# Performance work log

Measured on AMD Instinct MI355X. Metric: run time of the kernel, lower is better.

Reference implementation:

```python
import jax, jax.numpy as jnp
import numpy as np

B, D, F = 2048, 512, 16384
K = 3
AUX_THR = 0.7
EPS = 1e-8


def setup_inputs() -> dict:
    key = jax.random.key(0)
    ks = jax.random.split(key, 14)
    sc_e = 1.0 / np.sqrt(D)
    sc_d = 1.0 / np.sqrt(F)
    return {
        "model_activations": jax.random.normal(ks[0], (B, D), jnp.float32),
        "We": jax.random.normal(ks[1], (F, D), jnp.float32) * sc_e,
        "be": jax.random.normal(ks[2], (F,), jnp.float32) * 0.01,
        "Wd": jax.random.normal(ks[3], (D, F), jnp.float32) * sc_d,
        "bd": jax.random.normal(ks[4], (D,), jnp.float32) * 0.01,
        "We1": jax.random.normal(ks[5], (F, D), jnp.float32) * sc_e,
        "be1": jax.random.normal(ks[6], (F,), jnp.float32) * 0.01,
        "Wd1": jax.random.normal(ks[7], (D, F), jnp.float32) * sc_d,
        "bd1": jax.random.normal(ks[8], (D,), jnp.float32) * 0.01,
        "We2": jax.random.normal(ks[9], (F, D), jnp.float32) * sc_e,
        "be2": jax.random.normal(ks[10], (F,), jnp.float32) * 0.01,
        "Wd2": jax.random.normal(ks[11], (D, F), jnp.float32) * sc_d,
        "bd2": jax.random.normal(ks[12], (D,), jnp.float32) * 0.01,
    }


def _forward(x, We, be, Wd, bd, We1, be1, Wd1, bd1, We2, be2, Wd2, bd2):
    # parent encoder + top-k scatter
    pre = x @ We.T + be                                   # [B, F]
    vals, idx = jax.lax.top_k(pre, K)                     # [B, K]
    sae = jnp.zeros_like(pre).at[jnp.arange(B)[:, None], idx].set(vals)

    # child routing
    pre1 = x @ We1.T + be1
    pre2 = x @ We2.T + be2
    sae_nz = sae != 0.0
    m1 = jnp.where(sae_nz, pre1, 0.0)
    m2 = jnp.where(sae_nz, pre2, 0.0)
    winners = m1 > m2
    fa1 = jnp.where(winners, m1, 0.0)
    fa2 = jnp.where(~winners, m2, 0.0)

    recon = (sae @ Wd.T + bd) + (fa1 @ Wd1.T + bd1) + (fa2 @ Wd2.T + bd2)

    # live-latent counts (as arrays, jit-friendly)
    n_parent = jnp.zeros((F,), jnp.float32).at[idx.reshape(-1)].set(1.0).sum().astype(jnp.int32)
    n_c1 = jnp.any(fa1 != 0, axis=0).sum().astype(jnp.int32)
    n_c2 = jnp.any(fa2 != 0, axis=0).sum().astype(jnp.int32)

    # auxiliary cosine loss, computed per-feature without materializing
    # the [B, D, F] scaled_parent / combined_weights tensors:
    #   scaled_parent[b,:,f] = a * Wd[:,f],  scaled_child[b,:,f] = c * Wc[:,f]
    # cos over D reduces to per-feature Gram terms.
    pp = jnp.sum(Wd * Wd, axis=0)      # [F] ||Wp_f||^2
    p1 = jnp.sum(Wd * Wd1, axis=0)     # [F] Wp_f . W1_f
    p2 = jnp.sum(Wd * Wd2, axis=0)
    s11 = jnp.sum(Wd1 * Wd1, axis=0)
    s22 = jnp.sum(Wd2 * Wd2, axis=0)

    a = sae                                              # [B, F]
    c = jnp.where(winners, fa1, fa2)                     # [B, F]
    pc = jnp.where(winners, p1[None, :], p2[None, :])    # [B, F]
    cc = jnp.where(winners, s11[None, :], s22[None, :])

    dot = a * (a * pp[None, :] + c * pc)                 # <scaled_parent, combined>
    nx = jnp.abs(a) * jnp.sqrt(pp)[None, :]              # ||scaled_parent||
    ny2 = a * a * pp[None, :] + 2.0 * a * c * pc + c * c * cc
    ny = jnp.sqrt(jnp.maximum(ny2, 0.0))                 # ||combined||
    cos = dot / (jnp.maximum(nx, EPS) * jnp.maximum(ny, EPS))

    active = (a > 0).astype(cos.dtype)
    sim_loss = jnp.maximum(0.0, AUX_THR - cos) * active
    aux = sim_loss.sum() / (active.sum() + 1e-08)

    return recon, (n_parent, n_c1, n_c2), aux


def reference(model_activations, We, be, Wd, bd, We1, be1, Wd1, bd1, We2, be2, Wd2, bd2):
    return _forward(model_activations, We, be, Wd, bd, We1, be1, Wd1, bd1, We2, be2, Wd2, bd2)
```

## Files before the change

kernel.cpp:

```cpp
#include <hip/hip_runtime.h>
#include <math.h>

#define B_DIM 2048
#define D_DIM 512
#define F_DIM 16384
#define K_TOP 3

typedef __attribute__((ext_vector_type(8))) short bf16x8;
typedef __attribute__((ext_vector_type(4))) float f32x4;

#define GL16(gsrc, ldst) \
  __builtin_amdgcn_global_load_lds( \
      (__attribute__((address_space(1))) const void*)(gsrc), \
      (__attribute__((address_space(3))) void*)(ldst), 16, 0, 0)

__device__ __forceinline__ bool better(float v, int c, float w, int j) {
    return (v > w) || (v == w && c < j);
}

__device__ __forceinline__ void ins3(float v, int c,
    float& v0, int& i0, float& v1, int& i1, float& v2, int& i2)
{
    if (!better(v, c, v2, i2)) return;
    if (better(v, c, v1, i1)) {
        v2 = v1; i2 = i1;
        if (better(v, c, v0, i0)) { v1 = v0; i1 = i0; v0 = v; i0 = c; }
        else { v1 = v; i1 = c; }
    } else { v2 = v; i2 = c; }
}

__device__ __forceinline__ uint okey(uint b16, int col) {
    uint m = 0x8000u + ((b16 >> 15) * 0x7FFFu);
    return ((b16 ^ m) << 14) | (uint)(16383 - col);
}

__device__ __forceinline__ void insK8(uint k, uint* V) {
#pragma unroll
    for (int j = 0; j < 8; ++j) {
        uint hi = V[j] > k ? V[j] : k;
        uint lo = V[j] > k ? k : V[j];
        V[j] = hi; k = lo;
    }
}

__device__ __forceinline__ void insK3(uint k, uint& V0, uint& V1, uint& V2) {
    uint h0 = V0 > k ? V0 : k, l0 = V0 > k ? k : V0; V0 = h0; k = l0;
    uint h1 = V1 > k ? V1 : k, l1 = V1 > k ? k : V1; V1 = h1; k = l1;
    V2 = V2 > k ? V2 : k;
}

__global__ __launch_bounds__(256) void convert_kernel(
    const float* __restrict__ src, ushort* __restrict__ dst, int n8)
{
    int i = blockIdx.x * 256 + threadIdx.x;
    const int stride = gridDim.x * 256;
    for (; i < n8; i += stride) {
        float4 a = ((const float4*)src)[i * 2];
        float4 b = ((const float4*)src)[i * 2 + 1];
        uint4 o;
        o.x = (__float_as_uint(a.y) & 0xFFFF0000u) | (__float_as_uint(a.x) >> 16);
        o.y = (__float_as_uint(a.w) & 0xFFFF0000u) | (__float_as_uint(a.z) >> 16);
        o.z = (__float_as_uint(b.y) & 0xFFFF0000u) | (__float_as_uint(b.x) >> 16);
        o.w = (__float_as_uint(b.w) & 0xFFFF0000u) | (__float_as_uint(b.z) >> 16);
        ((uint4*)dst)[i] = o;
    }
}

__global__ __launch_bounds__(256) void gemm_kernel(
    const ushort* __restrict__ xb, const ushort* __restrict__ web,
    const float* __restrict__ be, uint* __restrict__ packed)
{
    __shared__ __align__(16) ushort As[2][4096];
    __shared__ __align__(16) ushort Bs[2][4096];

    const int t = threadIdx.x;
    const int l = t & 63;
    const int w = t >> 6;
    const int wr = w >> 1, wc = w & 1;
    const int bm0 = blockIdx.y << 7;
    const int fn0 = blockIdx.x << 7;
    const int frow = l & 15;
    const int q = l >> 4;

    const int srow = t >> 2;
    const int sgr = (t & 3) ^ ((t >> 3) & 3);
    const int soff = sgr << 3;
    const ushort* gA0 = xb + (size_t)(bm0 + srow) * D_DIM + soff;
    const ushort* gA1 = xb + (size_t)(bm0 + 64 + srow) * D_DIM + soff;
    const ushort* gB0 = web + (size_t)(fn0 + srow) * D_DIM + soff;
    const ushort* gB1 = web + (size_t)(fn0 + 64 + srow) * D_DIM + soff;

#define STAGE(bufp, koff) do { \
    GL16(gA0 + (koff), (char*)As + (bufp) * 8192 + t * 16); \
    GL16(gA1 + (koff), (char*)As + (bufp) * 8192 + 4096 + t * 16); \
    GL16(gB0 + (koff), (char*)Bs + (bufp) * 8192 + t * 16); \
    GL16(gB1 + (koff), (char*)Bs + (bufp) * 8192 + 4096 + t * 16); \
} while (0)

    f32x4 acc[4][4];
#pragma unroll
    for (int m = 0; m < 4; ++m)
#pragma unroll
        for (int n = 0; n < 4; ++n) acc[m][n] = (f32x4)(0.f);

    STAGE(0, 0);
    __syncthreads();

    const int qs = (q ^ ((frow >> 1) & 3)) << 3;
    const int aoff = (wr * 64 + frow) * 32 + qs;
    const int boff = (wc * 64 + frow) * 32 + qs;

    int cur = 0;
    for (int t16 = 0; t16 < 16; ++t16) {
        const ushort* Ab = &As[0][0] + cur * 4096 + aoff;
        const ushort* Bb = &Bs[0][0] + cur * 4096 + boff;
        bf16x8 af[4], bfr[4];
#pragma unroll
        for (int m = 0; m < 4; ++m) af[m] = *(const bf16x8*)(Ab + m * 512);
#pragma unroll
        for (int n = 0; n < 4; ++n) bfr[n] = *(const bf16x8*)(Bb + n * 512);
        if (t16 < 15) STAGE(cur ^ 1, (t16 + 1) * 32);
#pragma unroll
        for (int m = 0; m < 4; ++m)
#pragma unroll
            for (int n = 0; n < 4; ++n)
                acc[m][n] = __builtin_amdgcn_mfma_f32_16x16x32_bf16(
                    af[m], bfr[n], acc[m][n], 0, 0, 0);
        __syncthreads();
        cur ^= 1;
    }
#undef STAGE

    float bias[4];
#pragma unroll
    for (int n = 0; n < 4; ++n) bias[n] = be[fn0 + wc * 64 + n * 16 + frow];

    const int colb = fn0 + wc * 64 + frow;
    const int rowbase = bm0 + wr * 64 + (q << 2);
    const int tile2 = (blockIdx.x << 1) + wc;
#pragma unroll
    for (int m = 0; m < 4; ++m) {
#pragma unroll
        for (int i = 0; i < 4; ++i) {
            uint V0 = 0, V1 = 0, V2 = 0;
#pragma unroll
            for (int n = 0; n < 4; ++n) {
                float v = acc[m][n][i] + bias[n];
                uint key = okey(__float_as_uint(v) >> 16, colb + n * 16);
                insK3(key, V0, V1, V2);
            }
#pragma unroll
            for (int mk = 1; mk <= 8; mk <<= 1) {
                uint o0 = (uint)__shfl_xor((int)V0, mk);
                uint o1 = (uint)__shfl_xor((int)V1, mk);
                uint o2 = (uint)__shfl_xor((int)V2, mk);
                insK3(o0, V0, V1, V2);
                insK3(o1, V0, V1, V2);
                insK3(o2, V0, V1, V2);
            }
            if (frow == 0) {
                uint* dp = packed + (size_t)(rowbase + m * 16 + i) * 768 + tile2 * 3;
                dp[0] = V0; dp[1] = V1; dp[2] = V2;
            }
        }
    }
}

__global__ __launch_bounds__(64) void merge_kernel(
    const uint* __restrict__ packed, int* __restrict__ c8i)
{
    const int row = blockIdx.x;
    const int l = threadIdx.x;
    const uint* p = packed + (size_t)row * 768;
    uint V[8] = {0, 0, 0, 0, 0, 0, 0, 0};
#pragma unroll
    for (int m = 0; m < 12; ++m) {
        uint k = p[l + (m << 6)];
        if (k > V[7]) insK8(k, V);
    }
#pragma unroll
    for (int mk = 1; mk < 64; mk <<= 1) {
        uint o[8];
#pragma unroll
        for (int j = 0; j < 8; ++j) o[j] = (uint)__shfl_xor((int)V[j], mk);
#pragma unroll
        for (int j = 0; j < 8; ++j)
            if (o[j] > V[7]) insK8(o[j], V);
    }
    if (l == 0) {
#pragma unroll
        for (int j = 0; j < 8; ++j)
            c8i[row * 8 + j] = 16383 - (int)(V[j] & 16383u);
    }
}

__global__ __launch_bounds__(512) void refine_kernel(
    const float* __restrict__ x, const float* __restrict__ We,
    const float* __restrict__ be, const int* __restrict__ c8i,
    float* __restrict__ vals, int* __restrict__ idxv)
{
    const int row = blockIdx.x;
    const int wv = threadIdx.x >> 6, l = threadIdx.x & 63;
    const int f = c8i[row * 8 + wv];
    const float* xr = x + (size_t)row * D_DIM;
    const float* wp = We + (size_t)f * D_DIM;
    float s = 0.f;
#pragma unroll
    for (int m = 0; m < 8; ++m) { int e = l + (m << 6); s = fmaf(xr[e], wp[e], s); }
#pragma unroll
    for (int mk = 1; mk < 64; mk <<= 1) s += __shfl_xor(s, mk);
    __shared__ float sv[8];
    __shared__ int si[8];
    if (l == 0) { sv[wv] = s + be[f]; si[wv] = f; }
    __syncthreads();
    if (threadIdx.x == 0) {
        float v0 = -INFINITY, v1 = -INFINITY, v2 = -INFINITY;
        int i0 = 0x7fffffff, i1 = 0x7fffffff, i2 = 0x7fffffff;
        for (int k = 0; k < 8; ++k) ins3(sv[k], si[k], v0, i0, v1, i1, v2, i2);
        vals[row * 3 + 0] = v0; idxv[row * 3 + 0] = i0;
        vals[row * 3 + 1] = v1; idxv[row * 3 + 1] = i1;
        vals[row * 3 + 2] = v2; idxv[row * 3 + 2] = i2;
    }
}

__global__ __launch_bounds__(512) void trgram_kernel(
    const float* __restrict__ Wd, const float* __restrict__ Wd1,
    const float* __restrict__ Wd2, ushort* __restrict__ WdT,
    ushort* __restrict__ Wd1T, ushort* __restrict__ Wd2T,
    float* __restrict__ gram)
{
    __shared__ float tA[64][65], tB[64][65], tC[64][65];
    __shared__ float gred[8][64][5];
    const int t = threadIdx.x;
    const int f0 = blockIdx.x << 6;
    const int wg = t >> 6;
    const int fl = t & 63;
    float pp = 0, p1 = 0, p2 = 0, s11 = 0, s22 = 0;

    for (int ch = 0; ch < 8; ++ch) {
        const int d0 = ch << 6;
        float a[8], b[8], c[8];
#pragma unroll
        for (int it = 0; it < 8; ++it) {
            int dl = (it << 3) + wg;
            size_t off = (size_t)(d0 + dl) * F_DIM + f0 + fl;
            a[it] = Wd[off]; b[it] = Wd1[off]; c[it] = Wd2[off];
        }
        if (ch) __syncthreads();
#pragma unroll
        for (int it = 0; it < 8; ++it) {
            pp  = fmaf(a[it], a[it], pp);
            p1  = fmaf(a[it], b[it], p1);
            p2  = fmaf(a[it], c[it], p2);
            s11 = fmaf(b[it], b[it], s11);
            s22 = fmaf(c[it], c[it], s22);
            int dl = (it << 3) + wg;
            tA[dl][fl] = a[it]; tB[dl][fl] = b[it]; tC[dl][fl] = c[it];
        }
        __syncthreads();
#pragma unroll
        for (int it = 0; it < 8; ++it) {
            int flw = (it << 3) + wg, dlw = fl;
            size_t doff = (size_t)(f0 + flw) * D_DIM + d0 + dlw;
            WdT[doff]  = (ushort)(__float_as_uint(tA[dlw][flw]) >> 16);
            Wd1T[doff] = (ushort)(__float_as_uint(tB[dlw][flw]) >> 16);
            Wd2T[doff] = (ushort)(__float_as_uint(tC[dlw][flw]) >> 16);
        }
    }
    gred[wg][fl][0] = pp;  gred[wg][fl][1] = p1; gred[wg][fl][2] = p2;
    gred[wg][fl][3] = s11; gred[wg][fl][4] = s22;
    __syncthreads();
    if (t < 64) {
        float g0 = 0, g1 = 0, g2 = 0, g3 = 0, g4 = 0;
#pragma unroll
        for (int g = 0; g < 8; ++g) {
            g0 += gred[g][t][0]; g1 += gred[g][t][1]; g2 += gred[g][t][2];
            g3 += gred[g][t][3]; g4 += gred[g][t][4];
        }
        gram[f0 + t] = g0;
        gram[F_DIM + f0 + t] = g1;
        gram[2 * F_DIM + f0 + t] = g2;
        gram[3 * F_DIM + f0 + t] = g3;
        gram[4 * F_DIM + f0 + t] = g4;
    }
}

__global__ __launch_bounds__(256) void child_kernel(
    const float* __restrict__ x,
    const float* __restrict__ We1, const float* __restrict__ be1,
    const float* __restrict__ We2, const float* __restrict__ be2,
    const float* __restrict__ vals, const int* __restrict__ idxv,
    float* __restrict__ cvals, int* __restrict__ wflag,
    int* __restrict__ flagP, int* __restrict__ flag1, int* __restrict__ flag2)
{
    const int pair = (blockIdx.x << 2) + (threadIdx.x >> 6);
    const int lane = threadIdx.x & 63;
    const int b = pair / 3;
    const int f = idxv[pair];
    const float a = vals[pair];
    const float* xb = x + (size_t)b * D_DIM;
    const float* w1 = We1 + (size_t)f * D_DIM;
    const float* w2 = We2 + (size_t)f * D_DIM;
    float s1 = 0.f, s2 = 0.f;
#pragma unroll
    for (int m = 0; m < 8; ++m) {
        int e = lane + (m << 6);
        float xv = xb[e];
        s1 = fmaf(xv, w1[e], s1);
        s2 = fmaf(xv, w2[e], s2);
    }
#pragma unroll
    for (int m = 1; m < 64; m <<= 1) { s1 += __shfl_xor(s1, m); s2 += __shfl_xor(s2, m); }
    if (lane == 0) {
        float p1v = s1 + be1[f];
        float p2v = s2 + be2[f];
        float m1 = (a != 0.f) ? p1v : 0.f;
        float m2 = (a != 0.f) ? p2v : 0.f;
        bool win = m1 > m2;
        float fa1 = win ? m1 : 0.f;
        float fa2 = win ? 0.f : m2;
        cvals[pair] = win ? fa1 : fa2;
        wflag[pair] = win ? 1 : 0;
        flagP[f] = 1;
        if (fa1 != 0.f) flag1[f] = 1;
        if (fa2 != 0.f) flag2[f] = 1;
    }
}

__global__ __launch_bounds__(512) void recon_kernel(
    const ushort* __restrict__ WdT, const float* __restrict__ bd,
    const ushort* __restrict__ Wd1T, const float* __restrict__ bd1,
    const ushort* __restrict__ Wd2T, const float* __restrict__ bd2,
    const float* __restrict__ vals, const int* __restrict__ idxv,
    const float* __restrict__ cvals, const int* __restrict__ wflag,
    float* __restrict__ out)
{
    const int b = blockIdx.x;
    const int d = threadIdx.x;
    float o = bd[d] + bd1[d] + bd2[d];
#pragma unroll
    for (int k = 0; k < 3; ++k) {
        const int p = b * 3 + k;
        const int f = idxv[p];
        const float a = vals[p];
        const float c = cvals[p];
        const int win = wflag[p];
        const size_t off = (size_t)f * D_DIM + d;
        o = fmaf(a, __uint_as_float((uint)WdT[off] << 16), o);
        if (c != 0.f) {
            const ushort* wt = win ? Wd1T : Wd2T;
            o = fmaf(c, __uint_as_float((uint)wt[off] << 16), o);
        }
    }
    out[(size_t)b * D_DIM + d] = o;
}

__global__ __launch_bounds__(256) void aux_kernel(
    const float* __restrict__ vals, const float* __restrict__ cvals,
    const int* __restrict__ wflag, const int* __restrict__ idxv,
    const float* __restrict__ gram,
    float* __restrict__ auxpart, float* __restrict__ cntpart)
{
    const int p = blockIdx.x * 256 + threadIdx.x;
    float term = 0.f, act = 0.f;
    {
        const float a = vals[p];
        const float c = cvals[p];
        const int win = wflag[p];
        const int f = idxv[p];
        const float pp = gram[f];
        const float pc = win ? gram[F_DIM + f] : gram[2 * F_DIM + f];
        const float cc = win ? gram[3 * F_DIM + f] : gram[4 * F_DIM + f];
        const float dot = a * (a * pp + c * pc);
        const float nx = fabsf(a) * sqrtf(pp);
        const float ny2 = a * a * pp + 2.f * a * c * pc + c * c * cc;
        const float ny = sqrtf(fmaxf(ny2, 0.f));
        const float cosv = dot / (fmaxf(nx, 1e-8f) * fmaxf(ny, 1e-8f));
        if (a > 0.f) { act = 1.f; term = fmaxf(0.f, 0.7f - cosv); }
    }
#pragma unroll
    for (int m = 1; m < 64; m <<= 1) { term += __shfl_xor(term, m); act += __shfl_xor(act, m); }
    __shared__ float st[2][4];
    const int w = threadIdx.x >> 6;
    if ((threadIdx.x & 63) == 0) { st[0][w] = term; st[1][w] = act; }
    __syncthreads();
    if (threadIdx.x == 0) {
        auxpart[blockIdx.x] = st[0][0] + st[0][1] + st[0][2] + st[0][3];
        cntpart[blockIdx.x] = st[1][0] + st[1][1] + st[1][2] + st[1][3];
    }
}

__global__ __launch_bounds__(256) void finalize_kernel(
    const int* __restrict__ flagP, const int* __restrict__ flag1,
    const int* __restrict__ flag2,
    const float* __restrict__ auxpart, const float* __restrict__ cntpart,
    float* __restrict__ out)
{
    const int t = threadIdx.x;
    int sp = 0, s1 = 0, s2 = 0;
    for (int f = t; f < F_DIM; f += 256) { sp += flagP[f]; s1 += flag1[f]; s2 += flag2[f]; }
#pragma unroll
    for (int m = 1; m < 64; m <<= 1) {
        sp += __shfl_xor(sp, m); s1 += __shfl_xor(s1, m); s2 += __shfl_xor(s2, m);
    }
    __shared__ int red[3][4];
    const int w = t >> 6;
    if ((t & 63) == 0) { red[0][w] = sp; red[1][w] = s1; red[2][w] = s2; }
    __syncthreads();
    if (t == 0) {
        float np_ = (float)(red[0][0] + red[0][1] + red[0][2] + red[0][3]);
        float n1_ = (float)(red[1][0] + red[1][1] + red[1][2] + red[1][3]);
        float n2_ = (float)(red[2][0] + red[2][1] + red[2][2] + red[2][3]);
        float asum = 0.f, acnt = 0.f;
        for (int i = 0; i < 24; ++i) { asum += auxpart[i]; acnt += cntpart[i]; }
        const size_t base = (size_t)B_DIM * D_DIM;
        out[base + 0] = np_;
        out[base + 1] = n1_;
        out[base + 2] = n2_;
        out[base + 3] = asum / (acnt + 1e-8f);
    }
}

extern "C" void kernel_launch(void* const* d_in, const int* in_sizes, int n_in,
                              void* d_out, int out_size, void* d_ws, size_t ws_size,
                              hipStream_t stream)
{
    (void)in_sizes; (void)n_in; (void)out_size; (void)ws_size;
    const float* x   = (const float*)d_in[0];
    const float* We  = (const float*)d_in[1];
    const float* be  = (const float*)d_in[2];
    const float* Wd  = (const float*)d_in[3];
    const float* bd  = (const float*)d_in[4];
    const float* We1 = (const float*)d_in[5];
    const float* be1 = (const float*)d_in[6];
    const float* Wd1 = (const float*)d_in[7];
    const float* bd1 = (const float*)d_in[8];
    const float* We2 = (const float*)d_in[9];
    const float* be2 = (const float*)d_in[10];
    const float* Wd2 = (const float*)d_in[11];
    const float* bd2 = (const float*)d_in[12];
    float* out = (float*)d_out;

    ushort* x_bf  = (ushort*)d_ws;
    ushort* We_bf = x_bf + (size_t)B_DIM * D_DIM;
    ushort* WdT   = We_bf + (size_t)F_DIM * D_DIM;
    ushort* Wd1T  = WdT + (size_t)F_DIM * D_DIM;
    ushort* Wd2T  = Wd1T + (size_t)F_DIM * D_DIM;
    uint*   packed = (uint*)(Wd2T + (size_t)F_DIM * D_DIM);
    float*  gram  = (float*)(packed + (size_t)B_DIM * 768);
    int*    flagP = (int*)(gram + 5 * F_DIM);
    int*    flag1 = flagP + F_DIM;
    int*    flag2 = flag1 + F_DIM;
    int*    c8i   = flag2 + F_DIM;
    float*  vals  = (float*)(c8i + B_DIM * 8);
    int*    idxv  = (int*)(vals + B_DIM * 3);
    float*  cvals = (float*)(idxv + B_DIM * 3);
    int*    wflag = (int*)(cvals + B_DIM * 3);
    float*  auxpart = (float*)(wflag + B_DIM * 3);
    float*  cntpart = auxpart + 24;

    hipMemsetAsync(flagP, 0, 3 * F_DIM * sizeof(int), stream);

    convert_kernel<<<2048, 256, 0, stream>>>(We, We_bf, F_DIM * D_DIM / 8);
    convert_kernel<<<256, 256, 0, stream>>>(x, x_bf, B_DIM * D_DIM / 8);

    dim3 g1(F_DIM / 128, B_DIM / 128);
    gemm_kernel<<<g1, 256, 0, stream>>>(x_bf, We_bf, be, packed);
    merge_kernel<<<B_DIM, 64, 0, stream>>>(packed, c8i);
    refine_kernel<<<B_DIM, 512, 0, stream>>>(x, We, be, c8i, vals, idxv);

    trgram_kernel<<<F_DIM / 64, 512, 0, stream>>>(
        Wd, Wd1, Wd2, WdT, Wd1T, Wd2T, gram);
    child_kernel<<<(B_DIM * K_TOP) / 4, 256, 0, stream>>>(
        x, We1, be1, We2, be2, vals, idxv, cvals, wflag, flagP, flag1, flag2);
    recon_kernel<<<B_DIM, 512, 0, stream>>>(
        WdT, bd, Wd1T, bd1, Wd2T, bd2, vals, idxv, cvals, wflag, out);
    aux_kernel<<<(B_DIM * K_TOP) / 256, 256, 0, stream>>>(
        vals, cvals, wflag, idxv, gram, auxpart, cntpart);
    finalize_kernel<<<1, 256, 0, stream>>>(flagP, flag1, flag2, auxpart, cntpart, out);
}
```

Before: 147.9 us.

## Fuse pipeline kernels to cut launches and co-schedule transpose with GEMM

Merges the two convert launches into one grid, and folds the decoder transpose/Gram kernel into the encoder GEMM launch as extra blocks so both run concurrently. Merge and refine become one kernel that passes candidates through shared memory. Child routing, reconstruction and the aux loss become one per-row kernel, with per-row partial sums reduced in finalize. This removes several launches and intermediate global buffers, at the cost of a mixed-role kernel whose shared-memory and register usage is set by the larger branch, and a transpose tile reduced to 32 rows.

```diff
diff --git a/kernel.cpp b/kernel.cpp
--- a/kernel.cpp
+++ b/kernel.cpp
@@ -49,11 +49,22 @@
     V2 = V2 > k ? V2 : k;
 }
 
+__device__ __forceinline__ float bf2f(ushort u) {
+    return __uint_as_float((uint)u << 16);
+}
+
 __global__ __launch_bounds__(256) void convert_kernel(
-    const float* __restrict__ src, ushort* __restrict__ dst, int n8)
-{
-    int i = blockIdx.x * 256 + threadIdx.x;
-    const int stride = gridDim.x * 256;
+    const float* __restrict__ We, ushort* __restrict__ We_bf,
+    const float* __restrict__ x, ushort* __restrict__ x_bf)
+{
+    const float* src; ushort* dst; int n8, i, stride;
+    if (blockIdx.x < 2048) {
+        src = We; dst = We_bf; n8 = F_DIM * D_DIM / 8;
+        i = blockIdx.x * 256 + threadIdx.x; stride = 2048 * 256;
+    } else {
+        src = x; dst = x_bf; n8 = B_DIM * D_DIM / 8;
+        i = (blockIdx.x - 2048) * 256 + threadIdx.x; stride = 256 * 256;
+    }
     for (; i < n8; i += stride) {
         float4 a = ((const float4*)src)[i * 2];
         float4 b = ((const float4*)src)[i * 2 + 1];
@@ -66,19 +77,98 @@
     }
 }
 
-__global__ __launch_bounds__(256) void gemm_kernel(
+__global__ __launch_bounds__(256) void mega_kernel(
     const ushort* __restrict__ xb, const ushort* __restrict__ web,
-    const float* __restrict__ be, uint* __restrict__ packed)
-{
-    __shared__ __align__(16) ushort As[2][4096];
-    __shared__ __align__(16) ushort Bs[2][4096];
-
+    const float* __restrict__ be, uint* __restrict__ packed,
+    const float* __restrict__ Wd, const float* __restrict__ Wd1,
+    const float* __restrict__ Wd2, ushort* __restrict__ WdT,
+    ushort* __restrict__ Wd1T, ushort* __restrict__ Wd2T,
+    float* __restrict__ gram)
+{
+    __shared__ __align__(16) char smem[32768];
     const int t = threadIdx.x;
+
+    if (blockIdx.x < 256) {
+        float* tA = (float*)smem;
+        float* tB = tA + 32 * 65;
+        float* tC = tB + 32 * 65;
+        float* gr = tC + 32 * 65;
+        const int f0 = blockIdx.x << 6;
+        const int fl = t & 63, dgrp = t >> 6;
+        const int flw = t >> 2, oct = t & 3;
+        float pp = 0, p1 = 0, p2 = 0, s11 = 0, s22 = 0;
+
+        for (int ch = 0; ch < 16; ++ch) {
+            const int d0 = ch << 5;
+            float a[8], b[8], c[8];
+#pragma unroll
+            for (int j = 0; j < 8; ++j) {
+                int dl = dgrp * 8 + j;
+                size_t off = (size_t)(d0 + dl) * F_DIM + f0 + fl;
+                a[j] = Wd[off]; b[j] = Wd1[off]; c[j] = Wd2[off];
+            }
+            if (ch) __syncthreads();
+#pragma unroll
+            for (int j = 0; j < 8; ++j) {
+                pp  = fmaf(a[j], a[j], pp);
+                p1  = fmaf(a[j], b[j], p1);
+                p2  = fmaf(a[j], c[j], p2);
+                s11 = fmaf(b[j], b[j], s11);
+                s22 = fmaf(c[j], c[j], s22);
+                int dl = dgrp * 8 + j;
+                tA[dl * 65 + fl] = a[j];
+                tB[dl * 65 + fl] = b[j];
+                tC[dl * 65 + fl] = c[j];
+            }
+            __syncthreads();
+            uint4 oa, ob, oc;
+            {
+                ushort ua[8], ub[8], uc[8];
+#pragma unroll
+                for (int j = 0; j < 8; ++j) {
+                    int dl = oct * 8 + j;
+                    ua[j] = (ushort)(__float_as_uint(tA[dl * 65 + flw]) >> 16);
+                    ub[j] = (ushort)(__float_as_uint(tB[dl * 65 + flw]) >> 16);
+                    uc[j] = (ushort)(__float_as_uint(tC[dl * 65 + flw]) >> 16);
+                }
+                oa = make_uint4(ua[0] | (ua[1] << 16), ua[2] | (ua[3] << 16),
+                                ua[4] | (ua[5] << 16), ua[6] | (ua[7] << 16));
+                ob = make_uint4(ub[0] | (ub[1] << 16), ub[2] | (ub[3] << 16),
+                                ub[4] | (ub[5] << 16), ub[6] | (ub[7] << 16));
+                oc = make_uint4(uc[0] | (uc[1] << 16), uc[2] | (uc[3] << 16),
+                                uc[4] | (uc[5] << 16), uc[6] | (uc[7] << 16));
+            }
+            size_t doff = (size_t)(f0 + flw) * D_DIM + d0 + oct * 8;
+            *(uint4*)&WdT[doff]  = oa;
+            *(uint4*)&Wd1T[doff] = ob;
+            *(uint4*)&Wd2T[doff] = oc;
+        }
+        __syncthreads();
+        gr[(0 * 4 + dgrp) * 64 + fl] = pp;
+        gr[(1 * 4 + dgrp) * 64 + fl] = p1;
+        gr[(2 * 4 + dgrp) * 64 + fl] = p2;
+        gr[(3 * 4 + dgrp) * 64 + fl] = s11;
+        gr[(4 * 4 + dgrp) * 64 + fl] = s22;
+        __syncthreads();
+        if (t < 64) {
+#pragma unroll
+            for (int s = 0; s < 5; ++s) {
+                float g = gr[(s * 4 + 0) * 64 + t] + gr[(s * 4 + 1) * 64 + t]
+                        + gr[(s * 4 + 2) * 64 + t] + gr[(s * 4 + 3) * 64 + t];
+                gram[s * F_DIM + f0 + t] = g;
+            }
+        }
+        return;
+    }
+
+    ushort* As = (ushort*)smem;
+    ushort* Bs = As + 8192;
+    const int g = blockIdx.x - 256;
     const int l = t & 63;
     const int w = t >> 6;
     const int wr = w >> 1, wc = w & 1;
-    const int bm0 = blockIdx.y << 7;
-    const int fn0 = blockIdx.x << 7;
+    const int bm0 = (g >> 7) << 7;
+    const int fn0 = (g & 127) << 7;
     const int frow = l & 15;
     const int q = l >> 4;
 
@@ -112,8 +202,8 @@
 
     int cur = 0;
     for (int t16 = 0; t16 < 16; ++t16) {
-        const ushort* Ab = &As[0][0] + cur * 4096 + aoff;
-        const ushort* Bb = &Bs[0][0] + cur * 4096 + boff;
+        const ushort* Ab = As + cur * 4096 + aoff;
+        const ushort* Bb = Bs + cur * 4096 + boff;
         bf16x8 af[4], bfr[4];
 #pragma unroll
         for (int m = 0; m < 4; ++m) af[m] = *(const bf16x8*)(Ab + m * 512);
@@ -137,7 +227,7 @@
 
     const int colb = fn0 + wc * 64 + frow;
     const int rowbase = bm0 + wr * 64 + (q << 2);
-    const int tile2 = (blockIdx.x << 1) + wc;
+    const int tile2 = ((g & 127) << 1) + wc;
 #pragma unroll
     for (int m = 0; m < 4; ++m) {
 #pragma unroll
@@ -166,42 +256,45 @@
     }
 }
 
-__global__ __launch_bounds__(64) void merge_kernel(
-    const uint* __restrict__ packed, int* __restrict__ c8i)
-{
+__global__ __launch_bounds__(512) void mergerefine_kernel(
+    const uint* __restrict__ packed,
+    const float* __restrict__ x, const float* __restrict__ We,
+    const float* __restrict__ be,
+    float* __restrict__ vals, int* __restrict__ idxv)
+{
+    __shared__ int sc8[8];
+    __shared__ float sv[8];
+    __shared__ int si[8];
     const int row = blockIdx.x;
-    const int l = threadIdx.x;
-    const uint* p = packed + (size_t)row * 768;
-    uint V[8] = {0, 0, 0, 0, 0, 0, 0, 0};
-#pragma unroll
-    for (int m = 0; m < 12; ++m) {
-        uint k = p[l + (m << 6)];
-        if (k > V[7]) insK8(k, V);
-    }
-#pragma unroll
-    for (int mk = 1; mk < 64; mk <<= 1) {
-        uint o[8];
-#pragma unroll
-        for (int j = 0; j < 8; ++j) o[j] = (uint)__shfl_xor((int)V[j], mk);
-#pragma unroll
-        for (int j = 0; j < 8; ++j)
-            if (o[j] > V[7]) insK8(o[j], V);
-    }
-    if (l == 0) {
-#pragma unroll
-        for (int j = 0; j < 8; ++j)
-            c8i[row * 8 + j] = 16383 - (int)(V[j] & 16383u);
-    }
-}
-
-__global__ __launch_bounds__(512) void refine_kernel(
-    const float* __restrict__ x, const float* __restrict__ We,
-    const float* __restrict__ be, const int* __restrict__ c8i,
-    float* __restrict__ vals, int* __restrict__ idxv)
-{
-    const int row = blockIdx.x;
-    const int wv = threadIdx.x >> 6, l = threadIdx.x & 63;
-    const int f = c8i[row * 8 + wv];
+    const int t = threadIdx.x;
+
+    if (t < 64) {
+        const uint* p = packed + (size_t)row * 768;
+        uint V[8] = {0, 0, 0, 0, 0, 0, 0, 0};
+#pragma unroll
+        for (int m = 0; m < 12; ++m) {
+            uint k = p[t + (m << 6)];
+            if (k > V[7]) insK8(k, V);
+        }
+#pragma unroll
+        for (int mk = 1; mk < 64; mk <<= 1) {
+            uint o[8];
+#pragma unroll
+            for (int j = 0; j < 8; ++j) o[j] = (uint)__shfl_xor((int)V[j], mk);
+#pragma unroll
+            for (int j = 0; j < 8; ++j)
+                if (o[j] > V[7]) insK8(o[j], V);
+        }
+        if (t == 0) {
+#pragma unroll
+            for (int j = 0; j < 8; ++j)
+                sc8[j] = 16383 - (int)(V[j] & 16383u);
+        }
+    }
+    __syncthreads();
+
+    const int wv = t >> 6, l = t & 63;
+    const int f = sc8[wv];
     const float* xr = x + (size_t)row * D_DIM;
     const float* wp = We + (size_t)f * D_DIM;
     float s = 0.f;
@@ -209,11 +302,9 @@
     for (int m = 0; m < 8; ++m) { int e = l + (m << 6); s = fmaf(xr[e], wp[e], s); }
 #pragma unroll
     for (int mk = 1; mk < 64; mk <<= 1) s += __shfl_xor(s, mk);
-    __shared__ float sv[8];
-    __shared__ int si[8];
     if (l == 0) { sv[wv] = s + be[f]; si[wv] = f; }
     __syncthreads();
-    if (threadIdx.x == 0) {
+    if (t == 0) {
         float v0 = -INFINITY, v1 = -INFINITY, v2 = -INFINITY;
         int i0 = 0x7fffffff, i1 = 0x7fffffff, i2 = 0x7fffffff;
         for (int k = 0; k < 8; ++k) ins3(sv[k], si[k], v0, i0, v1, i1, v2, i2);
@@ -223,171 +314,89 @@
     }
 }
 
-__global__ __launch_bounds__(512) void trgram_kernel(
-    const float* __restrict__ Wd, const float* __restrict__ Wd1,
-    const float* __restrict__ Wd2, ushort* __restrict__ WdT,
-    ushort* __restrict__ Wd1T, ushort* __restrict__ Wd2T,
-    float* __restrict__ gram)
-{
-    __shared__ float tA[64][65], tB[64][65], tC[64][65];
-    __shared__ float gred[8][64][5];
-    const int t = threadIdx.x;
-    const int f0 = blockIdx.x << 6;
-    const int wg = t >> 6;
-    const int fl = t & 63;
-    float pp = 0, p1 = 0, p2 = 0, s11 = 0, s22 = 0;
-
-    for (int ch = 0; ch < 8; ++ch) {
-        const int d0 = ch << 6;
-        float a[8], b[8], c[8];
-#pragma unroll
-        for (int it = 0; it < 8; ++it) {
-            int dl = (it << 3) + wg;
-            size_t off = (size_t)(d0 + dl) * F_DIM + f0 + fl;
-            a[it] = Wd[off]; b[it] = Wd1[off]; c[it] = Wd2[off];
-        }
-        if (ch) __syncthreads();
-#pragma unroll
-        for (int it = 0; it < 8; ++it) {
-            pp  = fmaf(a[it], a[it], pp);
-            p1  = fmaf(a[it], b[it], p1);
-            p2  = fmaf(a[it], c[it], p2);
-            s11 = fmaf(b[it], b[it], s11);
-            s22 = fmaf(c[it], c[it], s22);
-            int dl = (it << 3) + wg;
-            tA[dl][fl] = a[it]; tB[dl][fl] = b[it]; tC[dl][fl] = c[it];
-        }
-        __syncthreads();
-#pragma unroll
-        for (int it = 0; it < 8; ++it) {
-            int flw = (it << 3) + wg, dlw = fl;
-            size_t doff = (size_t)(f0 + flw) * D_DIM + d0 + dlw;
-            WdT[doff]  = (ushort)(__float_as_uint(tA[dlw][flw]) >> 16);
-            Wd1T[doff] = (ushort)(__float_as_uint(tB[dlw][flw]) >> 16);
-            Wd2T[doff] = (ushort)(__float_as_uint(tC[dlw][flw]) >> 16);
-        }
-    }
-    gred[wg][fl][0] = pp;  gred[wg][fl][1] = p1; gred[wg][fl][2] = p2;
-    gred[wg][fl][3] = s11; gred[wg][fl][4] = s22;
-    __syncthreads();
-    if (t < 64) {
-        float g0 = 0, g1 = 0, g2 = 0, g3 = 0, g4 = 0;
-#pragma unroll
-        for (int g = 0; g < 8; ++g) {
-            g0 += gred[g][t][0]; g1 += gred[g][t][1]; g2 += gred[g][t][2];
-            g3 += gred[g][t][3]; g4 += gred[g][t][4];
-        }
-        gram[f0 + t] = g0;
-        gram[F_DIM + f0 + t] = g1;
-        gram[2 * F_DIM + f0 + t] = g2;
-        gram[3 * F_DIM + f0 + t] = g3;
-        gram[4 * F_DIM + f0 + t] = g4;
-    }
-}
-
-__global__ __launch_bounds__(256) void child_kernel(
+__global__ __launch_bounds__(512) void cra_kernel(
     const float* __restrict__ x,
     const float* __restrict__ We1, const float* __restrict__ be1,
     const float* __restrict__ We2, const float* __restrict__ be2,
     const float* __restrict__ vals, const int* __restrict__ idxv,
-    float* __restrict__ cvals, int* __restrict__ wflag,
-    int* __restrict__ flagP, int* __restrict__ flag1, int* __restrict__ flag2)
-{
-    const int pair = (blockIdx.x << 2) + (threadIdx.x >> 6);
-    const int lane = threadIdx.x & 63;
-    const int b = pair / 3;
-    const int f = idxv[pair];
-    const float a = vals[pair];
-    const float* xb = x + (size_t)b * D_DIM;
-    const float* w1 = We1 + (size_t)f * D_DIM;
-    const float* w2 = We2 + (size_t)f * D_DIM;
-    float s1 = 0.f, s2 = 0.f;
-#pragma unroll
-    for (int m = 0; m < 8; ++m) {
-        int e = lane + (m << 6);
-        float xv = xb[e];
-        s1 = fmaf(xv, w1[e], s1);
-        s2 = fmaf(xv, w2[e], s2);
-    }
-#pragma unroll
-    for (int m = 1; m < 64; m <<= 1) { s1 += __shfl_xor(s1, m); s2 += __shfl_xor(s2, m); }
-    if (lane == 0) {
-        float p1v = s1 + be1[f];
-        float p2v = s2 + be2[f];
-        float m1 = (a != 0.f) ? p1v : 0.f;
-        float m2 = (a != 0.f) ? p2v : 0.f;
+    const float* __restrict__ gram,
+    const ushort* __restrict__ WdT, const float* __restrict__ bd,
+    const ushort* __restrict__ Wd1T, const float* __restrict__ bd1,
+    const ushort* __restrict__ Wd2T, const float* __restrict__ bd2,
+    int* __restrict__ flagP, int* __restrict__ flag1, int* __restrict__ flag2,
+    float* __restrict__ auxpart, float* __restrict__ cntpart,
+    float* __restrict__ out)
+{
+    __shared__ float sval[3], sdot[3][2], scv[3], sterm[3], sact[3];
+    __shared__ int sidx[3], swin[3];
+    const int b = blockIdx.x;
+    const int t = threadIdx.x;
+
+    if (t < 3) { sidx[t] = idxv[b * 3 + t]; sval[t] = vals[b * 3 + t]; }
+    __syncthreads();
+
+    const int w = t >> 6, l = t & 63;
+    if (w < 6) {
+        const int p = w >> 1, mt = w & 1;
+        const int f = sidx[p];
+        const float* wp = (mt ? We2 : We1) + (size_t)f * D_DIM;
+        const float* xr = x + (size_t)b * D_DIM;
+        float s = 0.f;
+#pragma unroll
+        for (int m = 0; m < 8; ++m) { int e = l + (m << 6); s = fmaf(xr[e], wp[e], s); }
+#pragma unroll
+        for (int mk = 1; mk < 64; mk <<= 1) s += __shfl_xor(s, mk);
+        if (l == 0) sdot[p][mt] = s + (mt ? be2 : be1)[f];
+    }
+    __syncthreads();
+
+    if (t < 3) {
+        const int p = t;
+        const float a = sval[p];
+        const int f = sidx[p];
+        float m1 = (a != 0.f) ? sdot[p][0] : 0.f;
+        float m2 = (a != 0.f) ? sdot[p][1] : 0.f;
         bool win = m1 > m2;
         float fa1 = win ? m1 : 0.f;
         float fa2 = win ? 0.f : m2;
-        cvals[pair] = win ? fa1 : fa2;
-        wflag[pair] = win ? 1 : 0;
+        float cv = win ? fa1 : fa2;
+        scv[p] = cv; swin[p] = win ? 1 : 0;
         flagP[f] = 1;
         if (fa1 != 0.f) flag1[f] = 1;
         if (fa2 != 0.f) flag2[f] = 1;
-    }
-}
-
-__global__ __launch_bounds__(512) void recon_kernel(
-    const ushort* __restrict__ WdT, const float* __restrict__ bd,
-    const ushort* __restrict__ Wd1T, const float* __restrict__ bd1,
-    const ushort* __restrict__ Wd2T, const float* __restrict__ bd2,
-    const float* __restrict__ vals, const int* __restrict__ idxv,
-    const float* __restrict__ cvals, const int* __restrict__ wflag,
-    float* __restrict__ out)
-{
-    const int b = blockIdx.x;
-    const int d = threadIdx.x;
-    float o = bd[d] + bd1[d] + bd2[d];
-#pragma unroll
-    for (int k = 0; k < 3; ++k) {
-        const int p = b * 3 + k;
-        const int f = idxv[p];
-        const float a = vals[p];
-        const float c = cvals[p];
-        const int win = wflag[p];
-        const size_t off = (size_t)f * D_DIM + d;
-        o = fmaf(a, __uint_as_float((uint)WdT[off] << 16), o);
-        if (c != 0.f) {
-            const ushort* wt = win ? Wd1T : Wd2T;
-            o = fmaf(c, __uint_as_float((uint)wt[off] << 16), o);
-        }
-    }
-    out[(size_t)b * D_DIM + d] = o;
-}
-
-__global__ __launch_bounds__(256) void aux_kernel(
-    const float* __restrict__ vals, const float* __restrict__ cvals,
-    const int* __restrict__ wflag, const int* __restrict__ idxv,
-    const float* __restrict__ gram,
-    float* __restrict__ auxpart, float* __restrict__ cntpart)
-{
-    const int p = blockIdx.x * 256 + threadIdx.x;
-    float term = 0.f, act = 0.f;
-    {
-        const float a = vals[p];
-        const float c = cvals[p];
-        const int win = wflag[p];
-        const int f = idxv[p];
         const float pp = gram[f];
         const float pc = win ? gram[F_DIM + f] : gram[2 * F_DIM + f];
         const float cc = win ? gram[3 * F_DIM + f] : gram[4 * F_DIM + f];
-        const float dot = a * (a * pp + c * pc);
+        const float dot = a * (a * pp + cv * pc);
         const float nx = fabsf(a) * sqrtf(pp);
-        const float ny2 = a * a * pp + 2.f * a * c * pc + c * c * cc;
+        const float ny2 = a * a * pp + 2.f * a * cv * pc + cv * cv * cc;
         const float ny = sqrtf(fmaxf(ny2, 0.f));
         const float cosv = dot / (fmaxf(nx, 1e-8f) * fmaxf(ny, 1e-8f));
-        if (a > 0.f) { act = 1.f; term = fmaxf(0.f, 0.7f - cosv); }
-    }
-#pragma unroll
-    for (int m = 1; m < 64; m <<= 1) { term += __shfl_xor(term, m); act += __shfl_xor(act, m); }
-    __shared__ float st[2][4];
-    const int w = threadIdx.x >> 6;
-    if ((threadIdx.x & 63) == 0) { st[0][w] = term; st[1][w] = act; }
-    __syncthreads();
-    if (threadIdx.x == 0) {
-        auxpart[blockIdx.x] = st[0][0] + st[0][1] + st[0][2] + st[0][3];
-        cntpart[blockIdx.x] = st[1][0] + st[1][1] + st[1][2] + st[1][3];
-    }
+        sterm[p] = (a > 0.f) ? fmaxf(0.f, 0.7f - cosv) : 0.f;
+        sact[p] = (a > 0.f) ? 1.f : 0.f;
+    }
+    __syncthreads();
+    if (t == 0) {
+        auxpart[b] = sterm[0] + sterm[1] + sterm[2];
+        cntpart[b] = sact[0] + sact[1] + sact[2];
+    }
+
+    const int d = t;
+    float o = bd[d] + bd1[d] + bd2[d];
+#pragma unroll
+    for (int k = 0; k < 3; ++k) {
+        const int f = sidx[k];
+        const float a = sval[k];
+        const float c = scv[k];
+        const int win = swin[k];
+        const size_t off = (size_t)f * D_DIM + d;
+        o = fmaf(a, bf2f(WdT[off]), o);
+        if (c != 0.f) {
+            const ushort* wt = win ? Wd1T : Wd2T;
+            o = fmaf(c, bf2f(wt[off]), o);
+        }
+    }
+    out[(size_t)b * D_DIM + d] = o;
 }
 
 __global__ __launch_bounds__(256) void finalize_kernel(
@@ -399,25 +408,32 @@
     const int t = threadIdx.x;
     int sp = 0, s1 = 0, s2 = 0;
     for (int f = t; f < F_DIM; f += 256) { sp += flagP[f]; s1 += flag1[f]; s2 += flag2[f]; }
+    float asum = 0.f, acnt = 0.f;
+    for (int i = t; i < B_DIM; i += 256) { asum += auxpart[i]; acnt += cntpart[i]; }
 #pragma unroll
     for (int m = 1; m < 64; m <<= 1) {
         sp += __shfl_xor(sp, m); s1 += __shfl_xor(s1, m); s2 += __shfl_xor(s2, m);
+        asum += __shfl_xor(asum, m); acnt += __shfl_xor(acnt, m);
     }
     __shared__ int red[3][4];
+    __shared__ float fred[2][4];
     const int w = t >> 6;
-    if ((t & 63) == 0) { red[0][w] = sp; red[1][w] = s1; red[2][w] = s2; }
+    if ((t & 63) == 0) {
+        red[0][w] = sp; red[1][w] = s1; red[2][w] = s2;
+        fred[0][w] = asum; fred[1][w] = acnt;
+    }
     __syncthreads();
     if (t == 0) {
         float np_ = (float)(red[0][0] + red[0][1] + red[0][2] + red[0][3]);
         float n1_ = (float)(red[1][0] + red[1][1] + red[1][2] + red[1][3]);
         float n2_ = (float)(red[2][0] + red[2][1] + red[2][2] + red[2][3]);
-        float asum = 0.f, acnt = 0.f;
-        for (int i = 0; i < 24; ++i) { asum += auxpart[i]; acnt += cntpart[i]; }
+        float as = fred[0][0] + fred[0][1] + fred[0][2] + fred[0][3];
+        float ac = fred[1][0] + fred[1][1] + fred[1][2] + fred[1][3];
         const size_t base = (size_t)B_DIM * D_DIM;
         out[base + 0] = np_;
         out[base + 1] = n1_;
         out[base + 2] = n2_;
-        out[base + 3] = asum / (acnt + 1e-8f);
+        out[base + 3] = as / (ac + 1e-8f);
     }
 }
 
@@ -451,31 +467,27 @@
     int*    flagP = (int*)(gram + 5 * F_DIM);
     int*    flag1 = flagP + F_DIM;
     int*    flag2 = flag1 + F_DIM;
-    int*    c8i   = flag2 + F_DIM;
-    float*  vals  = (float*)(c8i + B_DIM * 8);
+    float*  vals  = (float*)(flag2 + F_DIM);
     int*    idxv  = (int*)(vals + B_DIM * 3);
-    float*  cvals = (float*)(idxv + B_DIM * 3);
-    int*    wflag = (int*)(cvals + B_DIM * 3);
-    float*  auxpart = (float*)(wflag + B_DIM * 3);
-    float*  cntpart = auxpart + 24;
+    float*  auxpart = (float*)(idxv + B_DIM * 3);
+    float*  cntpart = auxpart + B_DIM;
 
     hipMemsetAsync(flagP, 0, 3 * F_DIM * sizeof(int), stream);
 
-    convert_kernel<<<2048, 256, 0, stream>>>(We, We_bf, F_DIM * D_DIM / 8);
-    convert_kernel<<<256, 256, 0, stream>>>(x, x_bf, B_DIM * D_DIM / 8);
-
-    dim3 g1(F_DIM / 128, B_DIM / 128);
-    gemm_kernel<<<g1, 256, 0, stream>>>(x_bf, We_bf, be, packed);
-    merge_kernel<<<B_DIM, 64, 0, stream>>>(packed, c8i);
-    refine_kernel<<<B_DIM, 512, 0, stream>>>(x, We, be, c8i, vals, idxv);
-
-    trgram_kernel<<<F_DIM / 64, 512, 0, stream>>>(
+    convert_kernel<<<2304, 256, 0, stream>>>(We, We_bf, x, x_bf);
+
+    mega_kernel<<<2304, 256, 0, stream>>>(
+        x_bf, We_bf, be, packed,
         Wd, Wd1, Wd2, WdT, Wd1T, Wd2T, gram);
-    child_kernel<<<(B_DIM * K_TOP) / 4, 256, 0, stream>>>(
-        x, We1, be1, We2, be2, vals, idxv, cvals, wflag, flagP, flag1, flag2);
-    recon_kernel<<<B_DIM, 512, 0, stream>>>(
-        WdT, bd, Wd1T, bd1, Wd2T, bd2, vals, idxv, cvals, wflag, out);
-    aux_kernel<<<(B_DIM * K_TOP) / 256, 256, 0, stream>>>(
-        vals, cvals, wflag, idxv, gram, auxpart, cntpart);
-    finalize_kernel<<<1, 256, 0, stream>>>(flagP, flag1, flag2, auxpart, cntpart, out);
-}
+
+    mergerefine_kernel<<<B_DIM, 512, 0, stream>>>(
+        packed, x, We, be, vals, idxv);
+
+    cra_kernel<<<B_DIM, 512, 0, stream>>>(
+        x, We1, be1, We2, be2, vals, idxv, gram,
+        WdT, bd, Wd1T, bd1, Wd2T, bd2,
+        flagP, flag1, flag2, auxpart, cntpart, out);
+
+    finalize_kernel<<<1, 256, 0, stream>>>(
+        flagP, flag1, flag2, auxpart, cntpart, out);
+}
```

Measured after the change: 152.6 us. 1.03x slower.
